# Kernel tuning notes

Hardware: AMD Instinct MI355X
Metric: run time of the kernel (lower is better)

Reference implementation:

```python
import jax, jax.numpy as jnp
import numpy as np
import math

D_MODEL = 512; NHEAD = 8; D_HEAD = 64; C_OUT = 64
SEQ_LEN = 1024; PRED_LEN = 256; K = 8; DIM_FF = 2048
LOW_FREQ = 1; EPS = 1e-5
BATCH = 8


def _next_fast_len(n):
    # smallest 5-smooth integer >= n (matches scipy.fftpack.next_fast_len)
    while True:
        m = n
        for p in (2, 3, 5):
            while m % p == 0:
                m //= p
        if m == 1:
            return n
        n += 1


def _conv1d_fft(f, g, n):
    # matches torch conv1d_fft with N == M == n along axis 1 (cross-correlation via conj)
    fast_len = _next_fast_len(2 * n - 1)
    Ff = jnp.fft.rfft(f, n=fast_len, axis=1)
    Fg = jnp.fft.rfft(g, n=fast_len, axis=1)
    out = jnp.fft.irfft(Ff * jnp.conj(Fg), n=fast_len, axis=1)
    out = jnp.roll(out, -1, axis=1)
    return out[:, fast_len - n:fast_len]


def _exp_smooth(values, sw, v0, aux_values=None):
    # values: (b,t,h,d); sw: (h,1); v0: (1,1,h,d or 1)
    b, t, h, d = values.shape
    alpha = jax.nn.sigmoid(sw)                        # (h,1)
    powers = jnp.arange(t, dtype=values.dtype)
    weight = (1.0 - alpha) * alpha ** powers[::-1]    # (h,t)
    init_w = alpha ** (powers + 1.0)                  # (h,t)
    weight = weight.T[None, :, :, None]               # (1,t,h,1)
    init_w = init_w.T[None, :, :, None]
    out = init_w * v0 + _conv1d_fft(values, weight, t)
    if aux_values is not None:
        aux_w = weight * (alpha / (1.0 - alpha))[None, None, :, :]
        out = out + _conv1d_fft(aux_values, aux_w, t)
    return out


def _layer_norm(x, g, b):
    mu = x.mean(-1, keepdims=True)
    var = ((x - mu) ** 2).mean(-1, keepdims=True)
    return (x - mu) * jax.lax.rsqrt(var + EPS) * g + b


def _fourier_season(x):
    b, t, d = x.shape
    xf = jnp.fft.rfft(x, axis=1)                      # (b, t//2+1, d) complex
    hi = xf.shape[1] - 1 if t % 2 == 0 else xf.shape[1]
    xf = xf[:, LOW_FREQ:hi]                           # (b, F, d)
    freqs = (jnp.arange(t // 2 + 1, dtype=x.dtype) / t)[LOW_FREQ:hi]
    # top-K frequencies per (batch, feature) by amplitude
    _, idx = jax.lax.top_k(jnp.abs(jnp.moveaxis(xf, 1, 2)), K)   # (b,d,K)
    idx = jnp.moveaxis(idx, 2, 1)                     # (b,K,d)
    x_sel = jnp.take_along_axis(xf, idx, axis=1)      # (b,K,d) complex
    f_sel = freqs[idx]                                # (b,K,d)
    # trig re-synthesis / extrapolation over t + PRED_LEN steps
    x_all = jnp.concatenate([x_sel, jnp.conj(x_sel)], axis=1)    # (b,2K,d)
    f_all = jnp.concatenate([f_sel, -f_sel], axis=1)[:, :, None, :]  # (b,2K,1,d)
    t_val = jnp.arange(t + PRED_LEN, dtype=x.dtype).reshape(1, 1, -1, 1)
    amp = (jnp.abs(x_all) / t)[:, :, None, :]
    phase = jnp.angle(x_all)[:, :, None, :]
    x_time = amp * jnp.cos(2.0 * math.pi * f_all * t_val + phase)  # (b,2K,T,d)
    return x_time.sum(axis=1)                         # (b, t+PRED_LEN, d)


def _growth_layer(x, z0, in_w, in_b, sw, v0, out_w, out_b):
    b, t, _ = x.shape
    v = (x @ in_w.T + in_b).reshape(b, t, NHEAD, D_HEAD)
    v = jnp.concatenate([jnp.broadcast_to(z0[None, None], (b, 1, NHEAD, D_HEAD)), v], axis=1)
    v = v[:, 1:] - v[:, :-1]                          # first differences, (b,t,h,dh)
    s = _exp_smooth(v, sw, v0)
    s = jnp.concatenate([jnp.broadcast_to(v0, (b, 1, NHEAD, D_HEAD)), s], axis=1)  # (b,t+1,h,dh)
    return s.reshape(b, t + 1, NHEAD * D_HEAD) @ out_w.T + out_b


def _level_layer(level, growth, season, sw, v0, gw, gb, spw, spb):
    b, t, _ = level.shape
    g = (growth @ gw.T + gb)[..., None]               # (b,t,c,1)
    s = (season @ spw.T + spb)[..., None]             # (b,t,c,1)
    l = level[..., None] - s
    out = _exp_smooth(l, sw, v0, aux_values=g)        # (b,t,c,1)
    return out[..., 0]


def _forward(res, level, gl_z0, gl_in_w, gl_in_b, gl_sw, gl_v0, gl_out_w, gl_out_b,
             ll_sw, ll_v0, ll_gw, ll_gb, ll_sw2, ll_sb, ff_w1, ff_w2,
             n1_g, n1_b, n2_g, n2_b):
    season = _fourier_season(res)                     # (b, t+P, d)
    res = res - season[:, :-PRED_LEN]
    growth = _growth_layer(res, gl_z0, gl_in_w, gl_in_b, gl_sw, gl_v0, gl_out_w, gl_out_b)  # (b,t+1,d)
    res = _layer_norm(res - growth[:, 1:], n1_g, n1_b)
    ff = jax.nn.sigmoid(res @ ff_w1.T) @ ff_w2.T      # Feedforward, activation='sigmoid', no bias
    res = _layer_norm(res + ff, n2_g, n2_b)
    level = _level_layer(level, growth[:, :-1], season[:, :-PRED_LEN],
                         ll_sw, ll_v0, ll_gw, ll_gb, ll_sw2, ll_sb)
    return res, level, growth, season


def setup_inputs() -> dict:
    key = jax.random.key(0)
    ks = jax.random.split(key, 16)
    f32 = jnp.float32
    rn = lambda k, shape, s=1.0: jax.random.normal(k, shape, dtype=f32) * s
    return {
        "res": rn(ks[0], (BATCH, SEQ_LEN, D_MODEL)),
        "level": rn(ks[1], (BATCH, SEQ_LEN, C_OUT)),
        "gl_z0": rn(ks[2], (NHEAD, D_HEAD)),
        "gl_in_w": rn(ks[3], (NHEAD * D_HEAD, D_MODEL), 0.02),
        "gl_in_b": jnp.zeros((NHEAD * D_HEAD,), f32),
        "gl_sw": rn(ks[4], (NHEAD, 1)),
        "gl_v0": rn(ks[5], (1, 1, NHEAD, D_HEAD)),
        "gl_out_w": rn(ks[6], (D_MODEL, NHEAD * D_HEAD), 0.02),
        "gl_out_b": jnp.zeros((D_MODEL,), f32),
        "ll_sw": rn(ks[7], (C_OUT, 1)),
        "ll_v0": rn(ks[8], (1, 1, C_OUT, 1)),
        "ll_gw": rn(ks[9], (C_OUT, D_MODEL), 0.02),
        "ll_gb": jnp.zeros((C_OUT,), f32),
        "ll_sw2": rn(ks[10], (C_OUT, D_MODEL), 0.02),
        "ll_sb": jnp.zeros((C_OUT,), f32),
        "ff_w1": rn(ks[11], (DIM_FF, D_MODEL), 0.02),
        "ff_w2": rn(ks[12], (D_MODEL, DIM_FF), 0.02),
        "n1_g": jnp.ones((D_MODEL,), f32),
        "n1_b": jnp.zeros((D_MODEL,), f32),
        "n2_g": jnp.ones((D_MODEL,), f32),
        "n2_b": jnp.zeros((D_MODEL,), f32),
    }


def reference(res, level, gl_z0, gl_in_w, gl_in_b, gl_sw, gl_v0, gl_out_w, gl_out_b,
              ll_sw, ll_v0, ll_gw, ll_gb, ll_sw2, ll_sb, ff_w1, ff_w2,
              n1_g, n1_b, n2_g, n2_b):
    return _forward(res, level, gl_z0, gl_in_w, gl_in_b, gl_sw, gl_v0, gl_out_w, gl_out_b,
                    ll_sw, ll_v0, ll_gw, ll_gb, ll_sw2, ll_sb, ff_w1, ff_w2,
                    n1_g, n1_b, n2_g, n2_b)
```

## Files before the change

### kernel.cpp

```cpp
#include <hip/hip_runtime.h>
#include <hip/hip_bf16.h>
#include <math.h>

#define B_ 8
#define T_ 1024
#define D_ 512
#define PRED 256
#define TP (T_ + PRED)
#define NH 8
#define DH 64
#define DFF 2048
#define CO 64
#define KSEL 8

typedef __hip_bfloat16 bf16;
using bf16x8 = __attribute__((ext_vector_type(8))) short;
using f32x4  = __attribute__((ext_vector_type(4))) float;

__device__ __forceinline__ void gload_lds16(const void* gp, void* lp) {
  __builtin_amdgcn_global_load_lds(
      (const __attribute__((address_space(1))) void*)gp,
      (__attribute__((address_space(3))) void*)lp, 16, 0, 0);
}

template <int N>
__device__ __forceinline__ void vm_wait() {
  if constexpr (N == 0)      asm volatile("s_waitcnt vmcnt(0)" ::: "memory");
  else if constexpr (N == 2) asm volatile("s_waitcnt vmcnt(2)" ::: "memory");
  else if constexpr (N == 4) asm volatile("s_waitcnt vmcnt(4)" ::: "memory");
  else if constexpr (N == 6) asm volatile("s_waitcnt vmcnt(6)" ::: "memory");
  else if constexpr (N == 8) asm volatile("s_waitcnt vmcnt(8)" ::: "memory");
  else static_assert(N == 0, "unsupported vmcnt literal");
}

__global__ __launch_bounds__(256) void k_transpose(const float* __restrict__ in, float* __restrict__ out) {
  __shared__ float tile[32][33];
  const int b = blockIdx.z;
  const int d0 = blockIdx.x * 32, t0 = blockIdx.y * 32;
  const int tx = threadIdx.x, ty = threadIdx.y;
  const float* src = in + ((size_t)b * T_ + t0) * D_ + d0;
#pragma unroll
  for (int i = 0; i < 32; i += 8) tile[ty + i][tx] = src[(size_t)(ty + i) * D_ + tx];
  __syncthreads();
  float* dst = out + ((size_t)b * D_ + d0) * T_ + t0;
#pragma unroll
  for (int i = 0; i < 32; i += 8) dst[(size_t)(ty + i) * T_ + tx] = tile[tx][ty + i];
}

__global__ __launch_bounds__(256) void k_fft_topk(const float* __restrict__ xt, float* __restrict__ comp) {
  __shared__ float2 bufA[2][512], bufB[2][512], tw[256];
  __shared__ float wvv[2][4];
  __shared__ int wkk[2][4];
  __shared__ int selk[2][KSEL];
  float* const mg0 = (float*)&bufA[0][0];
  float* const mg1 = (float*)&bufA[1][0];
  const int j = threadIdx.x;
  const size_t bd0 = (size_t)blockIdx.x * 2;
  {
    const float ang = -(6.283185307179586f / 512.0f) * (float)j;
    tw[j] = make_float2(__cosf(ang), __sinf(ang));
  }
  const float4 u0 = ((const float4*)(xt + bd0 * 1024))[j];
  const float4 u1 = ((const float4*)(xt + (bd0 + 1) * 1024))[j];
  bufA[0][2 * j] = make_float2(u0.x, u0.y); bufA[0][2 * j + 1] = make_float2(u0.z, u0.w);
  bufA[1][2 * j] = make_float2(u1.x, u1.y); bufA[1][2 * j + 1] = make_float2(u1.z, u1.w);
  __syncthreads();
#pragma unroll
  for (int st = 0; st < 9; ++st) {
    const int s = 1 << st, p = j >> st, q = j & (s - 1), m = 256 >> st;
    const int ia = q + s * p, ib = q + s * (p + m);
    const int oa = q + s * 2 * p, ob = q + s * (2 * p + 1);
    float2 a0, b0, a1, b1;
    if ((st & 1) == 0) { a0 = bufA[0][ia]; b0 = bufA[0][ib]; a1 = bufA[1][ia]; b1 = bufA[1][ib]; }
    else               { a0 = bufB[0][ia]; b0 = bufB[0][ib]; a1 = bufB[1][ia]; b1 = bufB[1][ib]; }
    const float2 w = tw[p << st];
    const float2 s0 = make_float2(a0.x + b0.x, a0.y + b0.y);
    const float ex0 = a0.x - b0.x, ey0 = a0.y - b0.y;
    const float2 d0 = make_float2(ex0 * w.x - ey0 * w.y, ex0 * w.y + ey0 * w.x);
    const float2 s1 = make_float2(a1.x + b1.x, a1.y + b1.y);
    const float ex1 = a1.x - b1.x, ey1 = a1.y - b1.y;
    const float2 d1 = make_float2(ex1 * w.x - ey1 * w.y, ex1 * w.y + ey1 * w.x);
    if ((st & 1) == 0) { bufB[0][oa] = s0; bufB[0][ob] = d0; bufB[1][oa] = s1; bufB[1][ob] = d1; }
    else               { bufA[0][oa] = s0; bufA[0][ob] = d0; bufA[1][oa] = s1; bufA[1][ob] = d1; }
    __syncthreads();
  }
#pragma unroll
  for (int u = 0; u < 2; ++u) {
    const int k = (u == 0) ? (j + 1) : (j + 257);
    if (k <= 511) {
#pragma unroll
      for (int sx = 0; sx < 2; ++sx) {
        const float2 zk = bufB[sx][k & 511];
        const float2 zm = bufB[sx][(512 - k) & 511];
        const float Ex = 0.5f * (zk.x + zm.x), Ey = 0.5f * (zk.y - zm.y);
        const float Ox = 0.5f * (zk.y + zm.y), Oy = 0.5f * (zm.x - zk.x);
        const float ang = -(6.283185307179586f / 1024.0f) * (float)k;
        const float cs = __cosf(ang), sn = __sinf(ang);
        const float Xr = Ex + cs * Ox - sn * Oy;
        const float Xi = Ey + cs * Oy + sn * Ox;
        ((sx == 0) ? mg0 : mg1)[k] = Xr * Xr + Xi * Xi;
      }
    }
  }
  if (j == 0) { mg0[0] = -1.0f; mg1[0] = -1.0f; }
  __syncthreads();
  const int lane = j & 63, wvi = j >> 6;
  for (int r = 0; r < KSEL; ++r) {
    float bv0 = mg0[j]; int bk0 = j;
    { const float t = mg0[j + 256]; if (t > bv0) { bv0 = t; bk0 = j + 256; } }
    float bv1 = mg1[j]; int bk1 = j;
    { const float t = mg1[j + 256]; if (t > bv1) { bv1 = t; bk1 = j + 256; } }
#pragma unroll
    for (int off = 32; off; off >>= 1) {
      const float ov0 = __shfl_down(bv0, off); const int ok0 = __shfl_down(bk0, off);
      if (ov0 > bv0 || (ov0 == bv0 && ok0 < bk0)) { bv0 = ov0; bk0 = ok0; }
      const float ov1 = __shfl_down(bv1, off); const int ok1 = __shfl_down(bk1, off);
      if (ov1 > bv1 || (ov1 == bv1 && ok1 < bk1)) { bv1 = ov1; bk1 = ok1; }
    }
    if (lane == 0) { wvv[0][wvi] = bv0; wkk[0][wvi] = bk0; wvv[1][wvi] = bv1; wkk[1][wvi] = bk1; }
    __syncthreads();
    if (lane == 0 && j < 128) {
      const int sx = j >> 6;
      float fv = wvv[sx][0];
      int fk = wkk[sx][0];
#pragma unroll
      for (int i = 1; i < 4; i++)
        if (wvv[sx][i] > fv || (wvv[sx][i] == fv && wkk[sx][i] < fk)) { fv = wvv[sx][i]; fk = wkk[sx][i]; }
      selk[sx][r] = fk;
      ((sx == 0) ? mg0 : mg1)[fk] = -2.0f;
    }
    __syncthreads();
  }
  if (j < 2 * KSEL) {
    const int sx = j >> 3, r = j & 7;
    const int k = selk[sx][r];
    const float2 zk = bufB[sx][k & 511];
    const float2 zm = bufB[sx][(512 - k) & 511];
    const float Ex = 0.5f * (zk.x + zm.x), Ey = 0.5f * (zk.y - zm.y);
    const float Ox = 0.5f * (zk.y + zm.y), Oy = 0.5f * (zm.x - zk.x);
    const float ang = -(6.283185307179586f / 1024.0f) * (float)k;
    const float cs = __cosf(ang), sn = __sinf(ang);
    const float Xr = Ex + cs * Ox - sn * Oy;
    const float Xi = Ey + cs * Oy + sn * Ox;
    float* o = comp + (bd0 + sx) * 24 + r * 3;
    o[0] = 2.0f * sqrtf(Xr * Xr + Xi * Xi) * (1.0f / 1024.0f);
    o[1] = (float)k;
    o[2] = atan2f(Xi, Xr);
  }
}

__global__ __launch_bounds__(512) void k_season(const float* __restrict__ comp, const float* __restrict__ res,
                                                float* __restrict__ season, bf16* __restrict__ res1b,
                                                bf16* __restrict__ seasb) {
  const int d = threadIdx.x;
  const int b = blockIdx.y;
  const int t0 = blockIdx.x * 5;
  float a_[8], kf_[8], ph_[8];
  const float* c = comp + ((size_t)b * 512 + d) * 24;
#pragma unroll
  for (int i = 0; i < 8; i++) { a_[i] = c[3 * i]; kf_[i] = c[3 * i + 1]; ph_[i] = c[3 * i + 2]; }
#pragma unroll
  for (int tt = 0; tt < 5; ++tt) {
    const int t = t0 + tt;
    float acc = 0.0f;
#pragma unroll
    for (int i = 0; i < 8; i++) {
      float fr = kf_[i] * (float)t * (1.0f / 1024.0f);
      fr -= floorf(fr);
      acc += a_[i] * __cosf(fmaf(6.283185307179586f, fr, ph_[i]));
    }
    season[((size_t)b * TP + t) * D_ + d] = acc;
    if (t < T_) {
      const float rr = res[((size_t)b * T_ + t) * D_ + d] - acc;
      res1b[((size_t)b * T_ + t) * D_ + d] = __float2bfloat16(rr);
      seasb[((size_t)b * T_ + t) * D_ + d] = __float2bfloat16(acc);
    }
  }
}

#define CVT_TOTAL 2686976
__global__ __launch_bounds__(256) void k_cvt_all(const float* __restrict__ s0, const float* __restrict__ s1,
                                                 const float* __restrict__ s2_, const float* __restrict__ s3,
                                                 const float* __restrict__ s4, const float* __restrict__ s5,
                                                 bf16* __restrict__ dst) {
  const int i = (blockIdx.x * 256 + threadIdx.x) * 4;
  if (i >= CVT_TOTAL) return;
  const float* src;
  int off;
  if (i < 262144)       { src = s0;  off = i; }
  else if (i < 524288)  { src = s1;  off = i - 262144; }
  else if (i < 1572864) { src = s2_; off = i - 524288; }
  else if (i < 2621440) { src = s3;  off = i - 1572864; }
  else if (i < 2654208) { src = s4;  off = i - 2621440; }
  else                  { src = s5;  off = i - 2654208; }
  const float4 v = *(const float4*)(src + off);
  bf16* o = dst + i;
  o[0] = __float2bfloat16(v.x); o[1] = __float2bfloat16(v.y);
  o[2] = __float2bfloat16(v.z); o[3] = __float2bfloat16(v.w);
}

__global__ __launch_bounds__(1024) void k_growth_scan2(const float* __restrict__ v, const float* __restrict__ z0,
                                                       const float* __restrict__ sw, const float* __restrict__ v0,
                                                       bf16* __restrict__ s2) {
  const int b = blockIdx.x >> 3;
  const int col = (blockIdx.x & 7) * 64 + (threadIdx.x & 63);
  const int w = threadIdx.x >> 6;
  const float alpha = 1.0f / (1.0f + expf(-sw[col >> 6]));
  const float om = 1.0f - alpha;
  float a64 = alpha;
#pragma unroll
  for (int i = 0; i < 6; i++) a64 *= a64;
  const float* vp = v + (size_t)b * T_ * D_ + col;
  float vprev = (w == 0) ? z0[col] : vp[(size_t)(64 * w - 1) * D_];
  float sloc = 0.0f;
#pragma unroll 8
  for (int j = 0; j < 64; j++) {
    const float nv = vp[(size_t)(64 * w + j) * D_];
    sloc = alpha * sloc + om * (nv - vprev);
    vprev = nv;
  }
  __shared__ float lb[16][64], lc[16][64];
  lb[w][threadIdx.x & 63] = sloc;
  __syncthreads();
  if (w == 0) {
    float s = v0[col];
#pragma unroll
    for (int k = 0; k < 16; k++) { lc[k][threadIdx.x & 63] = s; s = a64 * s + lb[k][threadIdx.x & 63]; }
  }
  __syncthreads();
  float s = lc[w][threadIdx.x & 63];
  vprev = (w == 0) ? z0[col] : vp[(size_t)(64 * w - 1) * D_];
  bf16* op = s2 + (size_t)b * (T_ + 1) * D_ + col;
  if (w == 0) op[0] = __float2bfloat16(v0[col]);
#pragma unroll 8
  for (int j = 0; j < 64; j++) {
    const float nv = vp[(size_t)(64 * w + j) * D_];
    s = alpha * s + om * (nv - vprev);
    vprev = nv;
    op[(size_t)(64 * w + j + 1) * D_] = __float2bfloat16(s);
  }
}

__global__ __launch_bounds__(1024) void k_level_scan2(const float* __restrict__ level, const float* __restrict__ gp,
                                                      const float* __restrict__ sp, const float* __restrict__ sw,
                                                      const float* __restrict__ v0, float* __restrict__ out) {
  const int b = blockIdx.x;
  const int w = threadIdx.x >> 6;
  const int c = threadIdx.x & 63;
  const float alpha = 1.0f / (1.0f + expf(-sw[c]));
  const float om = 1.0f - alpha;
  float a64 = alpha;
#pragma unroll
  for (int i = 0; i < 6; i++) a64 *= a64;
  const size_t base = ((size_t)b * T_ + 64 * w) * CO + c;
  float sloc = 0.0f;
#pragma unroll 8
  for (int j = 0; j < 64; j++) {
    const size_t idx = base + (size_t)j * CO;
    const float u = om * (level[idx] - sp[idx]) + alpha * gp[idx];
    out[idx] = u;
    sloc = alpha * sloc + u;
  }
  __shared__ float lb[16][64], lc[16][64];
  lb[w][c] = sloc;
  __syncthreads();
  if (w == 0) {
    float s = v0[c];
#pragma unroll
    for (int k = 0; k < 16; k++) { lc[k][c] = s; s = a64 * s + lb[k][c]; }
  }
  __syncthreads();
  float s = lc[w][c];
#pragma unroll 8
  for (int j = 0; j < 64; j++) {
    const size_t idx = base + (size_t)j * CO;
    s = alpha * s + out[idx];
    out[idx] = s;
  }
}

template <int MODE>
__global__ __launch_bounds__(128) void k_ln(const float* __restrict__ x1, const float* __restrict__ x2,
                                            const float* __restrict__ x3, const float* __restrict__ g,
                                            const float* __restrict__ be, float* __restrict__ outF,
                                            bf16* __restrict__ outB) {
  const int m = blockIdx.x, tid = threadIdx.x;
  const int b = m >> 10;
  float4 v = ((const float4*)(x1 + (size_t)m * D_))[tid];
  if (MODE == 0) {
    const float4 se = ((const float4*)(x2 + ((size_t)(m + b * PRED)) * D_))[tid];
    const float4 gr = ((const float4*)(x3 + ((size_t)(m + b + 1)) * D_))[tid];
    v.x -= se.x + gr.x; v.y -= se.y + gr.y; v.z -= se.z + gr.z; v.w -= se.w + gr.w;
  }
  float s = v.x + v.y + v.z + v.w;
  float s2 = v.x * v.x + v.y * v.y + v.z * v.z + v.w * v.w;
#pragma unroll
  for (int off = 32; off; off >>= 1) { s += __shfl_down(s, off); s2 += __shfl_down(s2, off); }
  __shared__ float p1[2], p2[2];
  if ((tid & 63) == 0) { p1[tid >> 6] = s; p2[tid >> 6] = s2; }
  __syncthreads();
  const float S = p1[0] + p1[1], S2 = p2[0] + p2[1];
  const float mu = S * (1.0f / 512.0f);
  const float rs = rsqrtf(fmaxf(S2 * (1.0f / 512.0f) - mu * mu, 0.0f) + 1e-5f);
  const float4 gg = ((const float4*)g)[tid], bb = ((const float4*)be)[tid];
  float4 o;
  o.x = (v.x - mu) * rs * gg.x + bb.x;
  o.y = (v.y - mu) * rs * gg.y + bb.y;
  o.z = (v.z - mu) * rs * gg.z + bb.z;
  o.w = (v.w - mu) * rs * gg.w + bb.w;
  ((float4*)(outF + (size_t)m * D_))[tid] = o;
  if (MODE == 0) {
    bf16* ob = outB + (size_t)m * D_ + tid * 4;
    ob[0] = __float2bfloat16(o.x); ob[1] = __float2bfloat16(o.y);
    ob[2] = __float2bfloat16(o.z); ob[3] = __float2bfloat16(o.w);
  }
}

template <int BM, int BN, int BK, int WM, int WN, int EPI, bool DUAL = false>
__global__ __launch_bounds__(WM * WN * 64, 2) void k_gemm(
    const bf16* __restrict__ A, const bf16* __restrict__ Bw,
    const float* __restrict__ bias, float* outF, bf16* __restrict__ outB,
    const float* resid, const int M, const int N, const int K, int extra,
    const bf16* __restrict__ A2, const bf16* __restrict__ Bw2,
    const float* __restrict__ bias2, float* outF2, int extra2) {
  constexpr int NW = WM * WN;
  constexpr int FM = BM / (WM * 16);
  constexpr int FN = BN / (WN * 16);
  constexpr int RPC = 512 / BK;
  constexpr int LA = (BM / RPC) / NW, LB = (BN / RPC) / NW;
  constexpr int KK = BK / 32;
  constexpr int TLOADS = LA + LB;
  static_assert(LA >= 1 && LB >= 1, "tile too small for staging split");
  static_assert((BM / RPC) % NW == 0 && (BN / RPC) % NW == 0, "staging split");
  if constexpr (DUAL) {
    if (blockIdx.z == 1) { A = A2; Bw = Bw2; bias = bias2; outF = outF2; extra = extra2; }
  }
  __shared__ bf16 lsA[2][BM * BK];
  __shared__ bf16 lsB[2][BN * BK];
  const int tid = threadIdx.x;
  const int w = tid >> 6, lane = tid & 63;
  const int tm = blockIdx.x, tn = blockIdx.y;
  const int wr = w / WN, wc = w % WN;
  const int r16 = lane & 15, hi = lane >> 4;

  int srowoff, scoloff;
  if constexpr (BK == 64) {
    const int rr = lane >> 3, cs = lane & 7;
    srowoff = rr;
    scoloff = (cs ^ rr) * 8;
  } else {
    const int sr = lane >> 3, cs = lane & 7;
    const int idx = cs ^ (sr & 7);
    srowoff = sr * 2 + (idx >> 2);
    scoloff = (idx & 3) * 8;
  }

  const f32x4 fzero = {0.f, 0.f, 0.f, 0.f};
  f32x4 acc[FM][FN];
#pragma unroll
  for (int i = 0; i < FM; i++)
#pragma unroll
    for (int jj = 0; jj < FN; jj++) acc[i][jj] = fzero;

  const int NT = K / BK;

  auto stage = [&](int kt, int sel) {
#pragma unroll
    for (int q = 0; q < LA; q++) {
      const int g = w * LA + q;
      int m = tm * BM + g * RPC + srowoff;
      if (m > M - 1) m = M - 1;
      m += (m >> 10) * extra;
      gload_lds16(A + (size_t)m * K + (size_t)kt * BK + scoloff, &lsA[sel][g * 512]);
    }
#pragma unroll
    for (int q = 0; q < LB; q++) {
      const int g = w * LB + q;
      const int n = tn * BN + g * RPC + srowoff;
      gload_lds16(Bw + (size_t)n * K + (size_t)kt * BK + scoloff, &lsB[sel][g * 512]);
    }
  };

  auto frag = [&](const bf16* ls, int row, int cc) -> bf16x8 {
    if constexpr (BK == 64) {
      const int g = row >> 3, rr = row & 7;
      return *(const bf16x8*)&ls[g * 512 + rr * 64 + ((cc ^ rr) << 3)];
    } else {
      const int g = row >> 4, rr = row & 15, sr = rr >> 1;
      const int idx = ((rr & 1) << 2) | cc;
      return *(const bf16x8*)&ls[g * 512 + sr * 64 + ((idx ^ (sr & 7)) << 3)];
    }
  };

  stage(0, 0);
  for (int kt = 0; kt < NT; ++kt) {
    const int sel = kt & 1;
    if (kt + 1 < NT) {
      stage(kt + 1, sel ^ 1);
      vm_wait<TLOADS>();
    } else {
      vm_wait<0>();
    }
    __builtin_amdgcn_sched_barrier(0);
    __builtin_amdgcn_s_barrier();
    __builtin_amdgcn_sched_barrier(0);
#pragma unroll
    for (int kk = 0; kk < KK; ++kk) {
      bf16x8 af[FM], bfv[FN];
#pragma unroll
      for (int i = 0; i < FM; i++)
        af[i] = frag(lsA[sel], wr * (FM * 16) + i * 16 + r16, kk * 4 + hi);
#pragma unroll
      for (int jj = 0; jj < FN; jj++)
        bfv[jj] = frag(lsB[sel], wc * (FN * 16) + jj * 16 + r16, kk * 4 + hi);
#pragma unroll
      for (int i = 0; i < FM; i++)
#pragma unroll
        for (int jj = 0; jj < FN; jj++)
          acc[i][jj] = __builtin_amdgcn_mfma_f32_16x16x32_bf16(af[i], bfv[jj], acc[i][jj], 0, 0, 0);
    }
    if (kt + 1 < NT) {
      __builtin_amdgcn_sched_barrier(0);
      __builtin_amdgcn_s_barrier();
      __builtin_amdgcn_sched_barrier(0);
    }
  }

#pragma unroll
  for (int i = 0; i < FM; i++) {
#pragma unroll
    for (int r = 0; r < 4; r++) {
      const int m = tm * BM + wr * (FM * 16) + i * 16 + hi * 4 + r;
      if (m < M) {
#pragma unroll
        for (int jj = 0; jj < FN; jj++) {
          const int n = tn * BN + wc * (FN * 16) + jj * 16 + r16;
          float x = acc[i][jj][r];
          if (bias) x += bias[n];
          const size_t idx = (size_t)m * N + n;
          if (EPI == 0) {
            outF[idx] = x;
          } else if (EPI == 1) {
            outF[idx] = x;
            outB[idx] = __float2bfloat16(x);
          } else if (EPI == 2) {
            outB[idx] = __float2bfloat16(1.0f / (1.0f + __expf(-x)));
          } else {
            outF[idx] = x + resid[idx];
          }
        }
      }
    }
  }
}

#define MB (size_t)(1u << 20)
static const size_t OFF_A = 0;
static const size_t OFF_C = 32 * MB;
static const size_t OFF_D = 40 * MB;
static const size_t OFF_E = 48 * MB;
static const size_t OFF_F = 54 * MB;
static const size_t OFF_G = 63 * MB;
static const size_t OFF_H = 72 * MB;
static const size_t OFF_J = 88 * MB;
static const size_t OFF_K = 89 * MB;
static const size_t OFF_K2 = 91 * MB;

#define W_IN 0
#define W_OUT 262144
#define W_FF1 524288
#define W_FF2 1572864
#define W_GW 2621440
#define W_SW2 2654208

extern "C" void kernel_launch(void* const* d_in, const int* in_sizes, int n_in, void* d_out, int out_size,
                              void* d_ws, size_t ws_size, hipStream_t stream) {
  (void)in_sizes; (void)n_in; (void)out_size; (void)ws_size;
  const float* res = (const float*)d_in[0];
  const float* level = (const float*)d_in[1];
  const float* gl_z0 = (const float*)d_in[2];
  const float* gl_in_w = (const float*)d_in[3];
  const float* gl_in_b = (const float*)d_in[4];
  const float* gl_sw = (const float*)d_in[5];
  const float* gl_v0 = (const float*)d_in[6];
  const float* gl_out_w = (const float*)d_in[7];
  const float* gl_out_b = (const float*)d_in[8];
  const float* ll_sw = (const float*)d_in[9];
  const float* ll_v0 = (const float*)d_in[10];
  const float* ll_gw = (const float*)d_in[11];
  const float* ll_gb = (const float*)d_in[12];
  const float* ll_sw2 = (const float*)d_in[13];
  const float* ll_sb = (const float*)d_in[14];
  const float* ff_w1 = (const float*)d_in[15];
  const float* ff_w2 = (const float*)d_in[16];
  const float* n1_g = (const float*)d_in[17];
  const float* n1_b = (const float*)d_in[18];
  const float* n2_g = (const float*)d_in[19];
  const float* n2_b = (const float*)d_in[20];

  char* ws = (char*)d_ws;
  float* resT = (float*)(ws + OFF_A);
  float* vbuf = (float*)(ws + OFF_A);
  bf16* hbuf = (bf16*)(ws + OFF_A);
  bf16* res1b = (bf16*)(ws + OFF_C);
  bf16* res2b = (bf16*)(ws + OFF_C);
  bf16* seasb = (bf16*)(ws + OFF_D);
  bf16* wE = (bf16*)(ws + OFF_E);
  bf16* s2b = (bf16*)(ws + OFF_F);
  bf16* grob = (bf16*)(ws + OFF_G);
  float* res2f = (float*)(ws + OFF_H);
  float* comp = (float*)(ws + OFF_J);
  float* gproj = (float*)(ws + OFF_K);
  float* sproj = (float*)(ws + OFF_K2);

  float* o_res = (float*)d_out;
  float* o_level = o_res + 4194304;
  float* o_growth = o_level + 524288;
  float* o_season = o_growth + 4198400;

  k_transpose<<<dim3(16, 32, 8), dim3(32, 8), 0, stream>>>(res, resT);
  k_fft_topk<<<2048, 256, 0, stream>>>(resT, comp);
  k_season<<<dim3(256, 8), 512, 0, stream>>>(comp, res, o_season, res1b, seasb);
  k_cvt_all<<<(CVT_TOTAL / 4 + 255) / 256, 256, 0, stream>>>(gl_in_w, gl_out_w, ff_w1, ff_w2, ll_gw, ll_sw2, wE);
  k_gemm<64, 128, 64, 2, 2, 0><<<dim3(128, 4), 256, 0, stream>>>(
      res1b, wE + W_IN, gl_in_b, vbuf, nullptr, nullptr, 8192, 512, 512, 0,
      nullptr, nullptr, nullptr, nullptr, 0);
  k_growth_scan2<<<64, 1024, 0, stream>>>(vbuf, gl_z0, gl_sw, gl_v0, s2b);
  k_gemm<64, 128, 64, 2, 2, 1><<<dim3(129, 4), 256, 0, stream>>>(
      s2b, wE + W_OUT, gl_out_b, o_growth, grob, nullptr, 8200, 512, 512, 0,
      nullptr, nullptr, nullptr, nullptr, 0);
  k_ln<0><<<8192, 128, 0, stream>>>(res, o_season, o_growth, n1_g, n1_b, res2f, res2b);
  k_gemm<128, 128, 32, 2, 2, 2><<<dim3(64, 16), 256, 0, stream>>>(
      res2b, wE + W_FF1, nullptr, nullptr, hbuf, nullptr, 8192, 2048, 512, 0,
      nullptr, nullptr, nullptr, nullptr, 0);
  k_gemm<64, 128, 64, 2, 2, 3><<<dim3(128, 4), 256, 0, stream>>>(
      hbuf, wE + W_FF2, nullptr, res2f, nullptr, res2f, 8192, 512, 2048, 0,
      nullptr, nullptr, nullptr, nullptr, 0);
  k_ln<1><<<8192, 128, 0, stream>>>(res2f, nullptr, nullptr, n2_g, n2_b, o_res, nullptr);
  k_gemm<64, 64, 64, 4, 1, 0, true><<<dim3(128, 1, 2), 256, 0, stream>>>(
      grob, wE + W_GW, ll_gb, gproj, nullptr, nullptr, 8192, 64, 512, 1,
      seasb, wE + W_SW2, ll_sb, sproj, 0);
  k_level_scan2<<<8, 1024, 0, stream>>>(level, gproj, sproj, ll_sw, ll_v0, o_level);
}
```

Measured before the change: 220.0 us.

## Use radix-4 FFT, register-resident top-k, and bf16 residual input in LayerNorm

The 512-point FFT now runs one radix-2 stage followed by four radix-4 stages, which cuts the number of LDS round trips and barriers. The top-k selection keeps magnitudes in registers and double-buffers the per-wave partials, removing one barrier per round. The first LayerNorm reads the precomputed bf16 res-minus-season tensor instead of two fp32 tensors, which reduces memory traffic but lowers the precision of that input to bf16.

```diff
diff --git a/kernel.cpp b/kernel.cpp
--- a/kernel.cpp
+++ b/kernel.cpp
@@ -48,40 +48,64 @@
 }
 
 __global__ __launch_bounds__(256) void k_fft_topk(const float* __restrict__ xt, float* __restrict__ comp) {
-  __shared__ float2 bufA[2][512], bufB[2][512], tw[256];
-  __shared__ float wvv[2][4];
-  __shared__ int wkk[2][4];
+  __shared__ float2 bufA[2][512], bufB[2][512];
+  __shared__ float2 tw[384];
+  __shared__ float wvv[2][2][4];
+  __shared__ int wkk[2][2][4];
   __shared__ int selk[2][KSEL];
   float* const mg0 = (float*)&bufA[0][0];
   float* const mg1 = (float*)&bufA[1][0];
   const int j = threadIdx.x;
   const size_t bd0 = (size_t)blockIdx.x * 2;
   {
-    const float ang = -(6.283185307179586f / 512.0f) * (float)j;
-    tw[j] = make_float2(__cosf(ang), __sinf(ang));
+    const float c = -6.283185307179586f / 512.0f;
+    tw[j] = make_float2(__cosf(c * (float)j), __sinf(c * (float)j));
+    if (j < 128) tw[256 + j] = make_float2(__cosf(c * (float)(256 + j)), __sinf(c * (float)(256 + j)));
   }
   const float4 u0 = ((const float4*)(xt + bd0 * 1024))[j];
   const float4 u1 = ((const float4*)(xt + (bd0 + 1) * 1024))[j];
   bufA[0][2 * j] = make_float2(u0.x, u0.y); bufA[0][2 * j + 1] = make_float2(u0.z, u0.w);
   bufA[1][2 * j] = make_float2(u1.x, u1.y); bufA[1][2 * j + 1] = make_float2(u1.z, u1.w);
   __syncthreads();
-#pragma unroll
-  for (int st = 0; st < 9; ++st) {
-    const int s = 1 << st, p = j >> st, q = j & (s - 1), m = 256 >> st;
-    const int ia = q + s * p, ib = q + s * (p + m);
-    const int oa = q + s * 2 * p, ob = q + s * (2 * p + 1);
-    float2 a0, b0, a1, b1;
-    if ((st & 1) == 0) { a0 = bufA[0][ia]; b0 = bufA[0][ib]; a1 = bufA[1][ia]; b1 = bufA[1][ib]; }
-    else               { a0 = bufB[0][ia]; b0 = bufB[0][ib]; a1 = bufB[1][ia]; b1 = bufB[1][ib]; }
-    const float2 w = tw[p << st];
-    const float2 s0 = make_float2(a0.x + b0.x, a0.y + b0.y);
-    const float ex0 = a0.x - b0.x, ey0 = a0.y - b0.y;
-    const float2 d0 = make_float2(ex0 * w.x - ey0 * w.y, ex0 * w.y + ey0 * w.x);
-    const float2 s1 = make_float2(a1.x + b1.x, a1.y + b1.y);
-    const float ex1 = a1.x - b1.x, ey1 = a1.y - b1.y;
-    const float2 d1 = make_float2(ex1 * w.x - ey1 * w.y, ex1 * w.y + ey1 * w.x);
-    if ((st & 1) == 0) { bufB[0][oa] = s0; bufB[0][ob] = d0; bufB[1][oa] = s1; bufB[1][ob] = d1; }
-    else               { bufA[0][oa] = s0; bufA[0][ob] = d0; bufA[1][oa] = s1; bufA[1][ob] = d1; }
+  {
+    const float2 w = tw[j];
+#pragma unroll
+    for (int sx2 = 0; sx2 < 2; ++sx2) {
+      const float2 a = bufA[sx2][j], b = bufA[sx2][j + 256];
+      bufB[sx2][2 * j] = make_float2(a.x + b.x, a.y + b.y);
+      const float ex = a.x - b.x, ey = a.y - b.y;
+      bufB[sx2][2 * j + 1] = make_float2(ex * w.x - ey * w.y, ex * w.y + ey * w.x);
+    }
+  }
+  __syncthreads();
+  const int sx = j >> 7, idx = j & 127;
+#pragma unroll
+  for (int st = 0; st < 4; ++st) {
+    const int lg = 1 + 2 * st;
+    const int s = 1 << lg;
+    const int p = idx >> lg;
+    const int q = idx & (s - 1);
+    const float2* src = (st & 1) ? (const float2*)bufA[sx] : (const float2*)bufB[sx];
+    float2* dst = (st & 1) ? (float2*)bufB[sx] : (float2*)bufA[sx];
+    const float2 x0 = src[idx];
+    const float2 x1 = src[idx + 128];
+    const float2 x2 = src[idx + 256];
+    const float2 x3 = src[idx + 384];
+    const float2 e0 = make_float2(x0.x + x2.x, x0.y + x2.y);
+    const float2 e1 = make_float2(x0.x - x2.x, x0.y - x2.y);
+    const float2 e2 = make_float2(x1.x + x3.x, x1.y + x3.y);
+    const float2 e3 = make_float2(x1.x - x3.x, x1.y - x3.y);
+    const float2 y0 = make_float2(e0.x + e2.x, e0.y + e2.y);
+    const float2 y2 = make_float2(e0.x - e2.x, e0.y - e2.y);
+    const float2 y1 = make_float2(e1.x + e3.y, e1.y - e3.x);
+    const float2 y3 = make_float2(e1.x - e3.y, e1.y + e3.x);
+    const int spi = p << lg;
+    const float2 w1 = tw[spi], w2 = tw[2 * spi], w3 = tw[3 * spi];
+    const int ob = q + (p << (lg + 2));
+    dst[ob] = y0;
+    dst[ob + s] = make_float2(y1.x * w1.x - y1.y * w1.y, y1.x * w1.y + y1.y * w1.x);
+    dst[ob + 2 * s] = make_float2(y2.x * w2.x - y2.y * w2.y, y2.x * w2.y + y2.y * w2.x);
+    dst[ob + 3 * s] = make_float2(y3.x * w3.x - y3.y * w3.y, y3.x * w3.y + y3.y * w3.x);
     __syncthreads();
   }
 #pragma unroll
@@ -89,27 +113,30 @@
     const int k = (u == 0) ? (j + 1) : (j + 257);
     if (k <= 511) {
 #pragma unroll
-      for (int sx = 0; sx < 2; ++sx) {
-        const float2 zk = bufB[sx][k & 511];
-        const float2 zm = bufB[sx][(512 - k) & 511];
+      for (int s2 = 0; s2 < 2; ++s2) {
+        const float2 zk = bufB[s2][k & 511];
+        const float2 zm = bufB[s2][(512 - k) & 511];
         const float Ex = 0.5f * (zk.x + zm.x), Ey = 0.5f * (zk.y - zm.y);
         const float Ox = 0.5f * (zk.y + zm.y), Oy = 0.5f * (zm.x - zk.x);
         const float ang = -(6.283185307179586f / 1024.0f) * (float)k;
         const float cs = __cosf(ang), sn = __sinf(ang);
         const float Xr = Ex + cs * Ox - sn * Oy;
         const float Xi = Ey + cs * Oy + sn * Ox;
-        ((sx == 0) ? mg0 : mg1)[k] = Xr * Xr + Xi * Xi;
+        ((s2 == 0) ? mg0 : mg1)[k] = Xr * Xr + Xi * Xi;
       }
     }
   }
-  if (j == 0) { mg0[0] = -1.0f; mg1[0] = -1.0f; }
-  __syncthreads();
+  __syncthreads();
+  float a0 = mg0[j], b0v = mg0[j + 256];
+  float a1 = mg1[j], b1v = mg1[j + 256];
+  if (j == 0) { a0 = -1.0f; a1 = -1.0f; }
   const int lane = j & 63, wvi = j >> 6;
   for (int r = 0; r < KSEL; ++r) {
-    float bv0 = mg0[j]; int bk0 = j;
-    { const float t = mg0[j + 256]; if (t > bv0) { bv0 = t; bk0 = j + 256; } }
-    float bv1 = mg1[j]; int bk1 = j;
-    { const float t = mg1[j + 256]; if (t > bv1) { bv1 = t; bk1 = j + 256; } }
+    const int par = r & 1;
+    float bv0 = a0; int bk0 = j;
+    if (b0v > bv0) { bv0 = b0v; bk0 = j + 256; }
+    float bv1 = a1; int bk1 = j;
+    if (b1v > bv1) { bv1 = b1v; bk1 = j + 256; }
 #pragma unroll
     for (int off = 32; off; off >>= 1) {
       const float ov0 = __shfl_down(bv0, off); const int ok0 = __shfl_down(bk0, off);
@@ -117,32 +144,37 @@
       const float ov1 = __shfl_down(bv1, off); const int ok1 = __shfl_down(bk1, off);
       if (ov1 > bv1 || (ov1 == bv1 && ok1 < bk1)) { bv1 = ov1; bk1 = ok1; }
     }
-    if (lane == 0) { wvv[0][wvi] = bv0; wkk[0][wvi] = bk0; wvv[1][wvi] = bv1; wkk[1][wvi] = bk1; }
+    if (lane == 0) {
+      wvv[0][par][wvi] = bv0; wkk[0][par][wvi] = bk0;
+      wvv[1][par][wvi] = bv1; wkk[1][par][wvi] = bk1;
+    }
     __syncthreads();
-    if (lane == 0 && j < 128) {
-      const int sx = j >> 6;
-      float fv = wvv[sx][0];
-      int fk = wkk[sx][0];
-#pragma unroll
-      for (int i = 1; i < 4; i++)
-        if (wvv[sx][i] > fv || (wvv[sx][i] == fv && wkk[sx][i] < fk)) { fv = wvv[sx][i]; fk = wkk[sx][i]; }
-      selk[sx][r] = fk;
-      ((sx == 0) ? mg0 : mg1)[fk] = -2.0f;
-    }
-    __syncthreads();
-  }
+    float fv0 = wvv[0][par][0]; int fk0 = wkk[0][par][0];
+    float fv1 = wvv[1][par][0]; int fk1 = wkk[1][par][0];
+#pragma unroll
+    for (int i = 1; i < 4; i++) {
+      if (wvv[0][par][i] > fv0 || (wvv[0][par][i] == fv0 && wkk[0][par][i] < fk0)) { fv0 = wvv[0][par][i]; fk0 = wkk[0][par][i]; }
+      if (wvv[1][par][i] > fv1 || (wvv[1][par][i] == fv1 && wkk[1][par][i] < fk1)) { fv1 = wvv[1][par][i]; fk1 = wkk[1][par][i]; }
+    }
+    if (j == 0) { selk[0][r] = fk0; selk[1][r] = fk1; }
+    if (fk0 == j) a0 = -2.0f;
+    if (fk0 == j + 256) b0v = -2.0f;
+    if (fk1 == j) a1 = -2.0f;
+    if (fk1 == j + 256) b1v = -2.0f;
+  }
+  __syncthreads();
   if (j < 2 * KSEL) {
-    const int sx = j >> 3, r = j & 7;
-    const int k = selk[sx][r];
-    const float2 zk = bufB[sx][k & 511];
-    const float2 zm = bufB[sx][(512 - k) & 511];
+    const int s2 = j >> 3, r = j & 7;
+    const int k = selk[s2][r];
+    const float2 zk = bufB[s2][k & 511];
+    const float2 zm = bufB[s2][(512 - k) & 511];
     const float Ex = 0.5f * (zk.x + zm.x), Ey = 0.5f * (zk.y - zm.y);
     const float Ox = 0.5f * (zk.y + zm.y), Oy = 0.5f * (zm.x - zk.x);
     const float ang = -(6.283185307179586f / 1024.0f) * (float)k;
     const float cs = __cosf(ang), sn = __sinf(ang);
     const float Xr = Ex + cs * Ox - sn * Oy;
     const float Xi = Ey + cs * Oy + sn * Ox;
-    float* o = comp + (bd0 + sx) * 24 + r * 3;
+    float* o = comp + (bd0 + s2) * 24 + r * 3;
     o[0] = 2.0f * sqrtf(Xr * Xr + Xi * Xi) * (1.0f / 1024.0f);
     o[1] = (float)k;
     o[2] = atan2f(Xi, Xr);
@@ -280,17 +312,22 @@
 }
 
 template <int MODE>
-__global__ __launch_bounds__(128) void k_ln(const float* __restrict__ x1, const float* __restrict__ x2,
+__global__ __launch_bounds__(128) void k_ln(const float* __restrict__ x1, const bf16* __restrict__ xb,
                                             const float* __restrict__ x3, const float* __restrict__ g,
                                             const float* __restrict__ be, float* __restrict__ outF,
                                             bf16* __restrict__ outB) {
   const int m = blockIdx.x, tid = threadIdx.x;
   const int b = m >> 10;
-  float4 v = ((const float4*)(x1 + (size_t)m * D_))[tid];
+  float4 v;
   if (MODE == 0) {
-    const float4 se = ((const float4*)(x2 + ((size_t)(m + b * PRED)) * D_))[tid];
+    const ushort4 rb = ((const ushort4*)(xb + (size_t)m * D_))[tid];
     const float4 gr = ((const float4*)(x3 + ((size_t)(m + b + 1)) * D_))[tid];
-    v.x -= se.x + gr.x; v.y -= se.y + gr.y; v.z -= se.z + gr.z; v.w -= se.w + gr.w;
+    v.x = __uint_as_float((unsigned)rb.x << 16) - gr.x;
+    v.y = __uint_as_float((unsigned)rb.y << 16) - gr.y;
+    v.z = __uint_as_float((unsigned)rb.z << 16) - gr.z;
+    v.w = __uint_as_float((unsigned)rb.w << 16) - gr.w;
+  } else {
+    v = ((const float4*)(x1 + (size_t)m * D_))[tid];
   }
   float s = v.x + v.y + v.z + v.w;
   float s2 = v.x * v.x + v.y * v.y + v.z * v.z + v.w * v.w;
@@ -529,7 +566,7 @@
   k_gemm<64, 128, 64, 2, 2, 1><<<dim3(129, 4), 256, 0, stream>>>(
       s2b, wE + W_OUT, gl_out_b, o_growth, grob, nullptr, 8200, 512, 512, 0,
       nullptr, nullptr, nullptr, nullptr, 0);
-  k_ln<0><<<8192, 128, 0, stream>>>(res, o_season, o_growth, n1_g, n1_b, res2f, res2b);
+  k_ln<0><<<8192, 128, 0, stream>>>(nullptr, res1b, o_growth, n1_g, n1_b, res2f, res2b);
   k_gemm<128, 128, 32, 2, 2, 2><<<dim3(64, 16), 256, 0, stream>>>(
       res2b, wE + W_FF1, nullptr, nullptr, hbuf, nullptr, 8192, 2048, 512, 0,
       nullptr, nullptr, nullptr, nullptr, 0);
```

After: 216.4 us. Within noise of the previous version (-1.6%).
